# Kernel tuning notes

Hardware: AMD Instinct MI355X
Metric: run time of the kernel (lower is better)

## Reference

```python
import jax, jax.numpy as jnp
import numpy as np

LN_EPS = 1e-5
EPS = 1e-8
MESH_LR = 1.0
MESH_ITERS = 4
SH_ITERS = 5
SA_ITERS = 3


def build_grid(res):
    ranges = [np.linspace(0.0, 1.0, num=r) for r in res]
    g = np.stack(np.meshgrid(*ranges, indexing='ij'), axis=-1)
    g = g.reshape(res[0], res[1], -1)[None]
    return jnp.asarray(np.concatenate([g, 1.0 - g], axis=-1).astype(np.float32))  # [1,H,W,4]


def layer_norm(x, w, b):
    m = jnp.mean(x, axis=-1, keepdims=True)
    v = jnp.var(x, axis=-1, keepdims=True)
    return (x - m) * jax.lax.rsqrt(v + LN_EPS) * w + b


def l2norm(x):
    n = jnp.linalg.norm(x, axis=-1, keepdims=True)
    return x / jnp.maximum(n, 1e-12)  # matches F.normalize eps


def conv_relu(x, w, b, stride):
    y = jax.lax.conv_general_dilated(x, w, (stride, stride), [(2, 2), (2, 2)],
                                     dimension_numbers=('NCHW', 'OIHW', 'NCHW'))
    return jax.nn.relu(y + b[None, :, None, None])


def sinkhorn(C, a, b, u=None, v=None, n_iters=SH_ITERS):
    # log-domain Sinkhorn; C: [B,N,S] cost, a: [B,N], b: [B,S] marginals
    p = -C
    log_a, log_b = jnp.log(a), jnp.log(b)
    if u is None:
        u = jnp.zeros_like(a)
    if v is None:
        v = jnp.zeros_like(b)
    for _ in range(n_iters):
        u = log_a - jax.nn.logsumexp(p + v[:, None, :], axis=2)
        v = log_b - jax.nn.logsumexp(p + u[:, :, None], axis=1)
    pi = jnp.exp(p + u[:, :, None] + v[:, None, :])
    return pi, u, v


def minimize_entropy_of_sinkhorn(C0, a, b, mesh_lr=MESH_LR, n_mesh_iters=MESH_ITERS):
    # gradient descent on the cost matrix to minimize entropy of the transport plan
    def ent(C, u, v):
        pi, u2, v2 = sinkhorn(C, a, b, u=u, v=v)
        e = jnp.mean(-jnp.sum(pi * jnp.log(pi + EPS), axis=(1, 2)))
        return e, (u2, v2)

    grad_fn = jax.grad(ent, has_aux=True)
    u, v = jnp.zeros_like(a), jnp.zeros_like(b)
    C = C0
    for _ in range(n_mesh_iters):
        g, (u, v) = grad_fn(C, u, v)
        C = C - mesh_lr * g
    return C, u, v


def gru_cell(x, h, wih, whh, bih, bhh):
    gi = x @ wih.T + bih
    gh = h @ whh.T + bhh
    ir, iz, inn = jnp.split(gi, 3, axis=-1)
    hr, hz, hn = jnp.split(gh, 3, axis=-1)
    r = jax.nn.sigmoid(ir + hr)
    z = jax.nn.sigmoid(iz + hz)
    n = jnp.tanh(inn + r * hn)
    return (1.0 - z) * n + z * h


def setup_inputs() -> dict:
    key = jax.random.key(0)
    ks = iter(jax.random.split(key, 48))

    def nrm(shape, fan_in):
        return jax.random.normal(next(ks), shape, jnp.float32) / np.sqrt(fan_in).astype(np.float32)

    B, d, S, HID = 16, 64, 8, 128
    z = lambda *s: jnp.zeros(s, jnp.float32)
    o = lambda *s: jnp.ones(s, jnp.float32)
    inp = {
        'image': jax.random.normal(next(ks), (B, 3, 128, 128), jnp.float32),
        'slots_noise': jax.random.normal(next(ks), (B, S, d), jnp.float32),
        'conv1_w': nrm((64, 3, 5, 5), 75), 'conv1_b': z(64),
        'conv2_w': nrm((64, 64, 5, 5), 1600), 'conv2_b': z(64),
        'conv3_w': nrm((64, 64, 5, 5), 1600), 'conv3_b': z(64),
        'conv4_w': nrm((64, 64, 5, 5), 1600), 'conv4_b': z(64),
        'pos_w': nrm((d, 4), 4), 'pos_b': z(d),
        'mlp1_w': nrm((d, d), d), 'mlp1_b': z(d),
        'mlp2_w': nrm((d, d), d), 'mlp2_b': z(d),
        'ln_in_w': o(d), 'ln_in_b': z(d),
        'wk': nrm((d, d), d), 'wv': nrm((d, d), d), 'wq': nrm((d, d), d),
        'mwi_w': nrm((1, d), d), 'mwi_b': z(1),
        'mws_w': nrm((1, d), d), 'mws_b': z(1),
        'ln_sl_w': o(d), 'ln_sl_b': z(d),
        'gru_wih': nrm((3 * d, d), d), 'gru_whh': nrm((3 * d, d), d),
        'gru_bih': z(3 * d), 'gru_bhh': z(3 * d),
        'ln_ff_w': o(d), 'ln_ff_b': z(d),
        'fc1_w': nrm((HID, d), d), 'fc1_b': z(HID),
        'fc2_w': nrm((d, HID), HID), 'fc2_b': z(d),
        'slots_mu': nrm((1, 1, d), d),
        'slots_sigma': jax.random.uniform(next(ks), (1, 1, d), jnp.float32),
        'num_slots': 8,
    }
    return inp


def reference(image, slots_noise, conv1_w, conv1_b, conv2_w, conv2_b, conv3_w, conv3_b,
              conv4_w, conv4_b, pos_w, pos_b, mlp1_w, mlp1_b, mlp2_w, mlp2_b,
              ln_in_w, ln_in_b, wk, wv, wq, mwi_w, mwi_b, mws_w, mws_b,
              ln_sl_w, ln_sl_b, gru_wih, gru_whh, gru_bih, gru_bhh,
              ln_ff_w, ln_ff_b, fc1_w, fc1_b, fc2_w, fc2_b,
              slots_mu, slots_sigma, num_slots):
    B = image.shape[0]
    d = slots_mu.shape[-1]
    # --- CNN encoder (strided_convs=True => latent 32x32) ---
    x = conv_relu(image, conv1_w, conv1_b, 1)
    x = conv_relu(x, conv2_w, conv2_b, 2)
    x = conv_relu(x, conv3_w, conv3_b, 2)
    x = conv_relu(x, conv4_w, conv4_b, 1)          # [B,64,32,32]
    x = x.transpose(0, 2, 3, 1)                    # [B,32,32,64]
    grid = build_grid((32, 32))                    # [1,32,32,4]
    x = x + (grid @ pos_w.T + pos_b)               # soft position embed
    feat = x.reshape(B, -1, d)                     # [B,1024,64]
    # --- pre-slot-attention MLP ---
    feat = jax.nn.relu(feat @ mlp1_w.T + mlp1_b) @ mlp2_w.T + mlp2_b
    # --- slot attention with MESH-Sinkhorn ---
    n_s = num_slots
    slots = slots_mu + (jnp.abs(slots_sigma) + EPS) * slots_noise  # Normal rsample
    inp = layer_norm(feat, ln_in_w, ln_in_b)
    k = inp @ wk.T
    v = inp @ wv.T
    a = jax.nn.softmax((inp @ mwi_w.T + mwi_b).squeeze(-1), axis=-1) * n_s  # [B,N]
    kn = l2norm(k)
    attn = None
    for _ in range(SA_ITERS):
        slots_prev = slots
        s = layer_norm(slots, ln_sl_w, ln_sl_b)
        bm = jax.nn.softmax((s @ mws_w.T + mws_b).squeeze(-1), axis=-1) * n_s  # [B,S]
        q = s @ wq.T
        C = 1.0 - jnp.einsum('bnd,bsd->bns', kn, l2norm(q))  # cosine distance
        C, p, qq = minimize_entropy_of_sinkhorn(C, a, bm)
        pi, _, _ = sinkhorn(C, a, bm, u=p, v=qq)
        attn = pi.transpose(0, 2, 1)                         # [B,S,N]
        updates = jnp.einsum('bsn,bnd->bsd', attn, v)
        slots = gru_cell(updates.reshape(-1, d), slots_prev.reshape(-1, d),
                         gru_wih, gru_whh, gru_bih, gru_bhh).reshape(B, n_s, d)
        h = layer_norm(slots, ln_ff_w, ln_ff_b)
        slots = slots + (jax.nn.relu(h @ fc1_w.T + fc1_b) @ fc2_w.T + fc2_b)
    return slots, attn
```

## Files before the change

### kernel.cpp

```cpp
#include <hip/hip_runtime.h>
#include <hip/hip_bf16.h>


#define LN_EPS 1e-5f
#define SEPS 1e-8f
#define LN8 2.0794415416798357f

__device__ inline float ldf(float x) { return x; }
__device__ inline float ldf(__hip_bfloat16 x) { return __bfloat162float(x); }
__device__ inline void stf(float* p, float v) { *p = v; }
__device__ inline void stf(__hip_bfloat16* p, float v) { *p = __float2bfloat16(v); }

__device__ inline float wmaxall(float v) {
#pragma unroll
  for (int o = 32; o; o >>= 1) v = fmaxf(v, __shfl_down(v, o));
  return __shfl(v, 0);
}
__device__ inline float wsumall(float v) {
#pragma unroll
  for (int o = 32; o; o >>= 1) v += __shfl_down(v, o);
  return __shfl(v, 0);
}
__device__ inline int wsumi(int v) {
#pragma unroll
  for (int o = 32; o; o >>= 1) v += __shfl_down(v, o);
  return __shfl(v, 0);
}
__device__ inline float fast_sigmoid(float x) { return 1.f / (1.f + __expf(-x)); }
__device__ inline float fast_tanh(float x) { return 1.f - 2.f / (__expf(2.f * x) + 1.f); }

__global__ __launch_bounds__(64) void sniff_kernel(const unsigned int* __restrict__ img,
                                                   int* __restrict__ flag) {
  int cnt = 0;
  for (int i = threadIdx.x; i < 512; i += 64) {
    unsigned lo = img[i] & 0xFFFFu;
    int e = (int)((lo >> 7) & 0xFFu);
    cnt += (e >= 96 && e <= 140) ? 1 : 0;
  }
  cnt = wsumi(cnt);
  if (threadIdx.x == 0) *flag = (cnt >= 300) ? 1 : 0;
}

struct CvtArgs {
  const void* src[39];
  long off[40];
};

__global__ __launch_bounds__(256) void convert_kernel(CvtArgs a, const int* __restrict__ flag,
                                                      float* __restrict__ dst, long total) {
  const int isbf = *flag;
  for (long g = (long)blockIdx.x * 256 + threadIdx.x; g < total; g += (long)gridDim.x * 256) {
    int lo = 0, hi = 38;
    while (lo < hi) {
      int mid = (lo + hi + 1) >> 1;
      if (a.off[mid] <= g) lo = mid; else hi = mid - 1;
    }
    long li = g - a.off[lo];
    float v;
    if (isbf) v = __bfloat162float(((const __hip_bfloat16*)a.src[lo])[li]);
    else      v = ((const float*)a.src[lo])[li];
    dst[g] = v;
  }
}

struct TwArgs {
  long soff[9]; long doff[9]; int R[9]; int C[9];
};

__global__ __launch_bounds__(256) void transw_kernel(const float* __restrict__ cvt,
                                                     float* __restrict__ tws, TwArgs a) {
  int m = blockIdx.x;
  const float* S = cvt + a.soff[m];
  float* D = tws + a.doff[m];
  int R = a.R[m], C = a.C[m];
  for (int idx = threadIdx.x; idx < R * C; idx += 256) {
    int i = idx / C, j = idx - i * C;
    D[j * R + i] = S[idx];
  }
}

template <int S, typename TIN, typename TOUT>
__global__ __launch_bounds__(256) void conv5x5(
    const TIN* __restrict__ in, const float* __restrict__ wgt,
    const float* __restrict__ bias, TOUT* __restrict__ out,
    int Cin, int H, int W, int Ho, int Wo, int Cout, int tilesX) {
  constexpr int P = 15 * S + 5;
  constexpr int PP = (S == 1) ? 20 : 40;
  constexpr int NCH = (S == 1) ? 2 : 3;
  constexpr int NP = (P * P + 255) / 256;
  __shared__ __align__(16) float patch[P * PP];
  __shared__ float wt16[25 * 16];
  const int b = blockIdx.z;
  const int ocg = blockIdx.y * 16;
  const int ty0 = (blockIdx.x / tilesX) * 16, tx0 = (blockIdx.x % tilesX) * 16;
  const int og = threadIdx.x >> 6;
  const int r = (threadIdx.x >> 2) & 15;
  const int rx = threadIdx.x & 3;
  const int iy0 = ty0 * S - 2, ix0 = tx0 * S - 2;
  const long HW = (long)H * W;

  int toff[NP], soff[NP];
#pragma unroll
  for (int q = 0; q < NP; q++) {
    int idx = threadIdx.x + 256 * q;
    toff[q] = -1;
    soff[q] = -1;
    if (idx < P * P) {
      int py = idx / P, px = idx - py * P;
      int iy = iy0 + py, ix = ix0 + px;
      int pxs = (S == 2) ? (px ^ (((py >> 1) & 1) << 2)) : px;
      toff[q] = py * PP + pxs;
      if (iy >= 0 && iy < H && ix >= 0 && ix < W) soff[q] = iy * W + ix;
    }
  }
  int wsrc[2];
#pragma unroll
  for (int q = 0; q < 2; q++) {
    int idx = threadIdx.x + 256 * q;
    wsrc[q] = (idx < 400) ? (((ocg + (idx & 15)) * Cin) * 25 + (idx >> 4)) : -1;
  }

  float acc[4][4];
#pragma unroll
  for (int p = 0; p < 4; p++)
#pragma unroll
    for (int j = 0; j < 4; j++) acc[p][j] = 0.f;

  float pr[NP], wr[2];
  {
    const TIN* inp = in + (long)b * Cin * HW;
#pragma unroll
    for (int q = 0; q < NP; q++) pr[q] = (soff[q] >= 0) ? ldf(inp[soff[q]]) : 0.f;
#pragma unroll
    for (int q = 0; q < 2; q++) wr[q] = (wsrc[q] >= 0) ? wgt[wsrc[q]] : 0.f;
  }

  for (int ci = 0; ci < Cin; ++ci) {
    __syncthreads();
#pragma unroll
    for (int q = 0; q < NP; q++)
      if (toff[q] >= 0) patch[toff[q]] = pr[q];
#pragma unroll
    for (int q = 0; q < 2; q++) {
      int idx = threadIdx.x + 256 * q;
      if (idx < 400) wt16[idx] = wr[q];
    }
    __syncthreads();
    if (ci + 1 < Cin) {
      const TIN* inp = in + ((long)b * Cin + ci + 1) * HW;
#pragma unroll
      for (int q = 0; q < NP; q++) pr[q] = (soff[q] >= 0) ? ldf(inp[soff[q]]) : 0.f;
#pragma unroll
      for (int q = 0; q < 2; q++)
        if (wsrc[q] >= 0) wr[q] = wgt[wsrc[q] + (ci + 1) * 25];
    }
#pragma unroll
    for (int ky = 0; ky < 5; ky++) {
      float win[4 * NCH];
      const int row = r * S + ky;
      const float* rb = &patch[row * PP];
      if constexpr (S == 2) {
        const int sw = (row >> 1) & 1;
#pragma unroll
        for (int c = 0; c < NCH; c++) {
          const int g = rx * 2 + c;
          float4 t4 = *(const float4*)(rb + ((g ^ sw) << 2));
          win[4 * c + 0] = t4.x;
          win[4 * c + 1] = t4.y;
          win[4 * c + 2] = t4.z;
          win[4 * c + 3] = t4.w;
        }
      } else {
        const float* bp = rb + rx * 4;
#pragma unroll
        for (int c = 0; c < NCH; c++) {
          float4 t4 = *(const float4*)(bp + 4 * c);
          win[4 * c + 0] = t4.x;
          win[4 * c + 1] = t4.y;
          win[4 * c + 2] = t4.z;
          win[4 * c + 3] = t4.w;
        }
      }
#pragma unroll
      for (int kx = 0; kx < 5; kx++) {
        const float4 wv = *(const float4*)&wt16[(ky * 5 + kx) * 16 + og * 4];
#pragma unroll
        for (int p = 0; p < 4; p++) {
          float iv = win[p * S + kx];
          acc[p][0] += iv * wv.x;
          acc[p][1] += iv * wv.y;
          acc[p][2] += iv * wv.z;
          acc[p][3] += iv * wv.w;
        }
      }
    }
  }
  const int oy = ty0 + r, ox0 = tx0 + rx * 4;
#pragma unroll
  for (int j = 0; j < 4; j++) {
    int oc = ocg + og * 4 + j;
    float bs = bias[oc];
    TOUT* op = &out[(((long)b * Cout + oc) * Ho + oy) * Wo + ox0];
#pragma unroll
    for (int p = 0; p < 4; p++) stf(&op[p], fmaxf(acc[p][j] + bs, 0.f));
  }
}

__global__ __launch_bounds__(64) void token_kernel(
    const float* __restrict__ act4, const float* __restrict__ pos_w,
    const float* __restrict__ pos_b,
    const float* __restrict__ mlp1T, const float* __restrict__ mlp1_b,
    const float* __restrict__ mlp2T, const float* __restrict__ mlp2_b,
    const float* __restrict__ lnin_w, const float* __restrict__ lnin_b,
    const float* __restrict__ wkT, const float* __restrict__ wvT,
    const float* __restrict__ mwi_w, const float* __restrict__ mwi_b,
    float* __restrict__ knT_out, float* __restrict__ v_out, float* __restrict__ lg_out) {
  const int t = blockIdx.x, i = threadIdx.x;
  const int b = t >> 10, nn = t & 1023;
  const int h = nn >> 5, w = nn & 31;
  __shared__ float f[64], h1[64], inp[64];
  {
    float gh = h * (1.f / 31.f), gw = w * (1.f / 31.f);
    float e = gh * pos_w[i * 4 + 0] + gw * pos_w[i * 4 + 1] +
              (1.f - gh) * pos_w[i * 4 + 2] + (1.f - gw) * pos_w[i * 4 + 3] + pos_b[i];
    f[i] = act4[(((long)b * 64 + i) * 32 + h) * 32 + w] + e;
  }
  __syncthreads();
  float acc = 0.f;
  for (int j = 0; j < 64; j++) acc += f[j] * mlp1T[j * 64 + i];
  h1[i] = fmaxf(acc + mlp1_b[i], 0.f);
  __syncthreads();
  acc = 0.f;
  for (int j = 0; j < 64; j++) acc += h1[j] * mlp2T[j * 64 + i];
  float x = acc + mlp2_b[i];
  float m = wsumall(x) * (1.f / 64.f);
  float d0 = x - m;
  float var = wsumall(d0 * d0) * (1.f / 64.f);
  float xin = d0 * rsqrtf(var + LN_EPS) * lnin_w[i] + lnin_b[i];
  inp[i] = xin;
  __syncthreads();
  float kv = 0.f, vv = 0.f;
  for (int j = 0; j < 64; j++) {
    float ij = inp[j];
    kv += ij * wkT[j * 64 + i];
    vv += ij * wvT[j * 64 + i];
  }
  float ss = wsumall(kv * kv);
  knT_out[(long)b * 65536 + i * 1024 + nn] = kv / fmaxf(sqrtf(ss), 1e-12f);
  v_out[(long)t * 64 + i] = vv;
  float lg = wsumall(xin * mwi_w[i]);
  if (i == 0) lg_out[t] = lg + mwi_b[0];
}

__global__ __launch_bounds__(512) void sa_kernel(
    const float* __restrict__ knT_g, const float* __restrict__ v_g,
    const float* __restrict__ la_g, const float* __restrict__ noise,
    const float* __restrict__ mu_w, const float* __restrict__ sg_w,
    const float* __restrict__ lnsl_w, const float* __restrict__ lnsl_b,
    const float* __restrict__ mws_w, const float* __restrict__ mws_b,
    const float* __restrict__ wqT,
    const float* __restrict__ wihT, const float* __restrict__ whhT,
    const float* __restrict__ bih, const float* __restrict__ bhh,
    const float* __restrict__ lnff_w, const float* __restrict__ lnff_b,
    const float* __restrict__ fc1T, const float* __restrict__ fc1_b,
    const float* __restrict__ fc2T, const float* __restrict__ fc2_b,
    float* __restrict__ out) {
  const int b = blockIdx.x, tid = threadIdx.x;
  const int wv = tid >> 6, ln = tid & 63;

  __shared__ float sCt[8192];
  __shared__ float sEc[8192];
  __shared__ float sLa[1024], sELa[1024], sHid[1024];
  __shared__ float sPart[512 * 9];
  __shared__ float sVh[48], sV[8], sEsv[8], sGv[8], sLb[8], sBm[8];
  __shared__ float sC1[8], sEvh[8];
  __shared__ float sSlots[512], sNorm[512], sQn[512], sUpd[512];

  const float* knt = knT_g + (long)b * 65536;
  const float* vf = v_g + (long)b * 65536;
  float sInvH[5][2];
  float gPr[2][8];
  float gInit[2];

  {
    int dd = tid & 63;
    sSlots[tid] = mu_w[dd] + (fabsf(sg_w[dd]) + SEPS) * noise[(long)b * 512 + tid];
  }
  for (int n = tid; n < 1024; n += 512) sLa[n] = la_g[b * 1024 + n];
  __syncthreads();
  {
    float a0 = sLa[tid], a1 = sLa[tid + 512];
    float m0 = wmaxall(fmaxf(a0, a1));
    if (ln == 0) sBm[wv] = m0;
    __syncthreads();
    float M = sBm[0];
#pragma unroll
    for (int s = 1; s < 8; s++) M = fmaxf(M, sBm[s]);
    float e0 = wsumall(__expf(a0 - M) + __expf(a1 - M));
    if (ln == 0) sGv[wv] = e0;
    __syncthreads();
    float SS = 0.f;
#pragma unroll
    for (int s = 0; s < 8; s++) SS += sGv[s];
    float lse = M + __logf(SS);
    float l0 = a0 - lse + LN8, l1 = a1 - lse + LN8;
    sLa[tid] = l0;
    sLa[tid + 512] = l1;
    sELa[tid] = __expf(l0);
    sELa[tid + 512] = __expf(l1);
  }
  __syncthreads();

  for (int it = 0; it < 3; ++it) {
    {
      float x = sSlots[wv * 64 + ln];
      float m = wsumall(x) * (1.f / 64.f);
      float d0 = x - m;
      float var = wsumall(d0 * d0) * (1.f / 64.f);
      float xn = d0 * rsqrtf(var + LN_EPS) * lnsl_w[ln] + lnsl_b[ln];
      sNorm[wv * 64 + ln] = xn;
      float bmv = wsumall(xn * mws_w[ln]);
      if (ln == 0) sBm[wv] = bmv + mws_b[0];
    }
    __syncthreads();
    if (tid == 0) {
      float mx = -1e30f;
      for (int s = 0; s < 8; s++) mx = fmaxf(mx, sBm[s]);
      float ss = 0.f;
      for (int s = 0; s < 8; s++) ss += __expf(sBm[s] - mx);
      float lse = mx + __logf(ss);
      for (int s = 0; s < 8; s++) sLb[s] = sBm[s] - lse + LN8;
    }
    {
      float acc = 0.f;
      for (int j = 0; j < 64; j++) acc += sNorm[wv * 64 + j] * wqT[j * 64 + ln];
      sQn[tid] = acc;
    }
    __syncthreads();
    {
      float qv = sQn[wv * 64 + ln];
      float ss = wsumall(qv * qv);
      sQn[wv * 64 + ln] = qv / fmaxf(sqrtf(ss), 1e-12f);
    }
    if (tid < 8) {
      sV[tid] = 0.f;
      sEsv[tid] = 1.f;
    }
    __syncthreads();

#pragma unroll
    for (int k = 0; k < 2; k++) {
      int n = tid + 512 * k;
      float acc[8];
#pragma unroll
      for (int s = 0; s < 8; s++) acc[s] = 0.f;
      for (int j = 0; j < 64; j++) {
        float kvv = knt[j * 1024 + n];
#pragma unroll
        for (int s = 0; s < 8; s++) acc[s] += kvv * sQn[s * 64 + j];
      }
#pragma unroll
      for (int s = 0; s < 8; s++) {
        float c = 1.f - acc[s];
        sCt[s * 1024 + n] = c;
        sEc[s * 1024 + n] = __expf(-c);
      }
    }
    __syncthreads();

    for (int m = 0; m < 4; m++) {
#pragma unroll
      for (int t = 1; t <= 5; t++) {
        if (t == 1 && tid < 8) sVh[tid] = sV[tid];
        float esv_r[8], part[8];
#pragma unroll
        for (int s = 0; s < 8; s++) { esv_r[s] = sEsv[s]; part[s] = 0.f; }
#pragma unroll
        for (int k = 0; k < 2; k++) {
          int n = tid + 512 * k;
          float ec[8], S = 0.f;
#pragma unroll
          for (int s = 0; s < 8; s++) {
            ec[s] = sEc[s * 1024 + n];
            S += esv_r[s] * ec[s];
          }
          float inv = 1.f / S;
          sInvH[t - 1][k] = inv;
          float w = sELa[n] * inv;
#pragma unroll
          for (int s = 0; s < 8; s++) part[s] += w * ec[s];
        }
#pragma unroll
        for (int s = 0; s < 8; s++) sPart[tid * 9 + s] = part[s];
        __syncthreads();
        {
          int s = wv;
          float acc = 0.f;
#pragma unroll
          for (int q = 0; q < 8; q++) acc += sPart[(ln + 64 * q) * 9 + s];
          acc = wsumall(acc);
          if (ln == 0) {
            float vs = sLb[s] - __logf(acc);
            sV[s] = vs;
            sVh[t * 8 + s] = vs;
            sEsv[s] = __expf(vs);
          }
        }
        __syncthreads();
      }
      {
        float esv_r[8], part[8];
#pragma unroll
        for (int s = 0; s < 8; s++) { esv_r[s] = sEsv[s]; part[s] = 0.f; }
#pragma unroll
        for (int k = 0; k < 2; k++) {
          int n = tid + 512 * k;
          float al = sELa[n] * sInvH[4][k];
          float gul = 0.f;
#pragma unroll
          for (int s = 0; s < 8; s++) {
            float pi = al * esv_r[s] * sEc[s * 1024 + n];
            float gl = -(__logf(pi + SEPS) + pi / (pi + SEPS)) * pi * (1.f / 16.f);
            gPr[k][s] = gl;
            gul += gl;
            part[s] += gl;
          }
          gInit[k] = gul;
        }
#pragma unroll
        for (int s = 0; s < 8; s++) sPart[tid * 9 + s] = part[s];
        __syncthreads();
        {
          int s = wv;
          float acc = 0.f;
#pragma unroll
          for (int q = 0; q < 8; q++) acc += sPart[(ln + 64 * q) * 9 + s];
          acc = wsumall(acc);
          if (ln == 0) {
            sGv[s] = acc;
            sC1[s] = acc * __expf(sVh[40 + s] - sLb[s]);
            sEvh[s] = __expf(sVh[32 + s]);
          }
        }
        __syncthreads();
      }
#pragma unroll
      for (int t = 5; t >= 1; t--) {
        float c1_r[8], evh_r[8], part[8];
#pragma unroll
        for (int s = 0; s < 8; s++) {
          c1_r[s] = sC1[s];
          evh_r[s] = sEvh[s];
          part[s] = 0.f;
        }
#pragma unroll
        for (int k = 0; k < 2; k++) {
          int n = tid + 512 * k;
          float inv = sInvH[t - 1][k];
          float al = sELa[n] * inv;
          float gul = (t == 5) ? gInit[k] : 0.f;
          float ec[8];
#pragma unroll
          for (int s = 0; s < 8; s++) {
            ec[s] = sEc[s * 1024 + n];
            float t2 = al * c1_r[s] * ec[s];
            gPr[k][s] -= t2;
            gul -= t2;
          }
          float bv = gul * inv;
#pragma unroll
          for (int s = 0; s < 8; s++) {
            float pe = bv * ec[s];
            gPr[k][s] -= pe * evh_r[s];
            part[s] += pe;
          }
          if (t == 1) {
#pragma unroll
            for (int s = 0; s < 8; s++) {
              float cn = sCt[s * 1024 + n] + gPr[k][s];
              sCt[s * 1024 + n] = cn;
              sEc[s * 1024 + n] = __expf(-cn);
            }
          }
        }
        if (t > 1) {
#pragma unroll
          for (int s = 0; s < 8; s++) sPart[tid * 9 + s] = part[s];
        }
        if (t == 1 && tid < 8) {
          float vs = sVh[40 + tid];
          sV[tid] = vs;
          sEsv[tid] = __expf(vs);
        }
        __syncthreads();
        if (t > 1) {
          int s = wv;
          float acc = 0.f;
#pragma unroll
          for (int q = 0; q < 8; q++) acc += sPart[(ln + 64 * q) * 9 + s];
          acc = wsumall(acc);
          if (ln == 0) {
            float gn = -sEvh[s] * acc;
            sGv[s] = gn;
            sC1[s] = gn * __expf(sVh[(t - 1) * 8 + s] - sLb[s]);
            sEvh[s] = __expf(sVh[(t - 2) * 8 + s]);
          }
          __syncthreads();
        }
      }
    }

    float invF[2];
    for (int t = 0; t < 5; t++) {
      float esv_r[8], part[8];
#pragma unroll
      for (int s = 0; s < 8; s++) { esv_r[s] = sEsv[s]; part[s] = 0.f; }
#pragma unroll
      for (int k = 0; k < 2; k++) {
        int n = tid + 512 * k;
        float ec[8], S = 0.f;
#pragma unroll
        for (int s = 0; s < 8; s++) {
          ec[s] = sEc[s * 1024 + n];
          S += esv_r[s] * ec[s];
        }
        float inv = 1.f / S;
        invF[k] = inv;
        float w = sELa[n] * inv;
#pragma unroll
        for (int s = 0; s < 8; s++) part[s] += w * ec[s];
      }
#pragma unroll
      for (int s = 0; s < 8; s++) sPart[tid * 9 + s] = part[s];
      __syncthreads();
      {
        int s = wv;
        float acc = 0.f;
#pragma unroll
        for (int q = 0; q < 8; q++) acc += sPart[(ln + 64 * q) * 9 + s];
        acc = wsumall(acc);
        if (ln == 0) {
          float vs = sLb[s] - __logf(acc);
          sV[s] = vs;
          sEsv[s] = __expf(vs);
        }
      }
      __syncthreads();
    }
    {
      float esv_r[8];
#pragma unroll
      for (int s = 0; s < 8; s++) esv_r[s] = sEsv[s];
#pragma unroll
      for (int k = 0; k < 2; k++) {
        int n = tid + 512 * k;
        float al = sELa[n] * invF[k];
#pragma unroll
        for (int s = 0; s < 8; s++)
          sCt[s * 1024 + n] = al * esv_r[s] * sEc[s * 1024 + n];
      }
    }
    __syncthreads();
    if (it == 2) {
      for (int o = tid; o < 8192; o += 512) out[8192 + (long)b * 8192 + o] = sCt[o];
    }
    {
      int s = tid >> 6, dd = tid & 63;
      float acc = 0.f;
      for (int n = 0; n < 1024; n++) acc += sCt[s * 1024 + n] * vf[n * 64 + dd];
      sUpd[tid] = acc;
    }
    __syncthreads();
    float newslot;
    {
      int s = tid >> 6, i = tid & 63;
      const float* x = &sUpd[s * 64];
      const float* h = &sSlots[s * 64];
      float gir = 0, giz = 0, gin = 0, ghr = 0, ghz = 0, ghn = 0;
      for (int j = 0; j < 64; j++) {
        float xv = x[j], hv = h[j];
        gir += xv * wihT[j * 192 + i];
        giz += xv * wihT[j * 192 + 64 + i];
        gin += xv * wihT[j * 192 + 128 + i];
        ghr += hv * whhT[j * 192 + i];
        ghz += hv * whhT[j * 192 + 64 + i];
        ghn += hv * whhT[j * 192 + 128 + i];
      }
      gir += bih[i]; giz += bih[64 + i]; gin += bih[128 + i];
      ghr += bhh[i]; ghz += bhh[64 + i]; ghn += bhh[128 + i];
      float r = fast_sigmoid(gir + ghr);
      float z = fast_sigmoid(giz + ghz);
      float nn = fast_tanh(gin + r * ghn);
      newslot = (1.f - z) * nn + z * h[i];
    }
    __syncthreads();
    sSlots[tid] = newslot;
    __syncthreads();
    {
      float x = sSlots[wv * 64 + ln];
      float m = wsumall(x) * (1.f / 64.f);
      float d0 = x - m;
      float var = wsumall(d0 * d0) * (1.f / 64.f);
      sNorm[wv * 64 + ln] = d0 * rsqrtf(var + LN_EPS) * lnff_w[ln] + lnff_b[ln];
    }
    __syncthreads();
    for (int o = tid; o < 1024; o += 512) {
      int s = o >> 7, k2 = o & 127;
      float acc = 0.f;
      for (int j = 0; j < 64; j++) acc += sNorm[s * 64 + j] * fc1T[j * 128 + k2];
      sHid[o] = fmaxf(acc + fc1_b[k2], 0.f);
    }
    __syncthreads();
    {
      int s = tid >> 6, i = tid & 63;
      float acc = 0.f;
      for (int j = 0; j < 128; j++) acc += sHid[s * 128 + j] * fc2T[j * 64 + i];
      newslot = sSlots[tid] + acc + fc2_b[i];
    }
    __syncthreads();
    sSlots[tid] = newslot;
    __syncthreads();
  }
  out[(long)b * 512 + tid] = sSlots[tid];
}

extern "C" void kernel_launch(void* const* d_in, const int* in_sizes, int n_in,
                              void* d_out, int out_size, void* d_ws, size_t ws_size,
                              hipStream_t stream) {
  (void)n_in; (void)out_size; (void)ws_size;
  char* ws = (char*)d_ws;
  float* cvt  = (float*)ws;
  float* lgts = (float*)(ws + 5570560ull);
  __hip_bfloat16* act1 = (__hip_bfloat16*)(ws + 5636096ull);
  __hip_bfloat16* act2 = (__hip_bfloat16*)(ws + 39190528ull);
  float* act3 = (float*)(ws + 5636096ull);
  float* act4 = (float*)(ws + 9830400ull);
  float* knT  = (float*)(ws + 14024704ull);
  float* vf   = (float*)(ws + 18219008ull);
  int*   flag = (int*)(ws + 47579136ull);
  float* tws  = (float*)(ws + 47583232ull);

  CvtArgs ca;
  long total = 0;
  for (int i = 0; i < 39; i++) { ca.src[i] = d_in[i]; ca.off[i] = total; total += in_sizes[i]; }
  ca.off[39] = total;

  sniff_kernel<<<1, 64, 0, stream>>>((const unsigned int*)d_in[0], flag);
  convert_kernel<<<1024, 256, 0, stream>>>(ca, flag, cvt, total);

#define ARR(i) (cvt + ca.off[i])
  TwArgs ta;
  {
    const int src[9] = {12, 14, 18, 19, 20, 27, 28, 33, 35};
    const int R[9] = {64, 64, 64, 64, 64, 192, 192, 128, 64};
    const int C[9] = {64, 64, 64, 64, 64, 64, 64, 64, 128};
    long d = 0;
    for (int m2 = 0; m2 < 9; m2++) {
      ta.soff[m2] = ca.off[src[m2]];
      ta.doff[m2] = d;
      ta.R[m2] = R[m2];
      ta.C[m2] = C[m2];
      d += (long)R[m2] * C[m2];
    }
  }
  transw_kernel<<<9, 256, 0, stream>>>(cvt, tws, ta);
  float* mlp1T = tws + 0,     *mlp2T = tws + 4096,  *wkT = tws + 8192, *wvT = tws + 12288;
  float* wqT   = tws + 16384, *wihT  = tws + 20480, *whhT = tws + 32768;
  float* fc1T  = tws + 45056, *fc2T  = tws + 53248;

  const float* image = ARR(0);
  const float* noise = ARR(1);

  conv5x5<1, float, __hip_bfloat16><<<dim3(64, 4, 16), 256, 0, stream>>>(
      image, ARR(2), ARR(3), act1, 3, 128, 128, 128, 128, 64, 8);
  conv5x5<2, __hip_bfloat16, __hip_bfloat16><<<dim3(16, 4, 16), 256, 0, stream>>>(
      act1, ARR(4), ARR(5), act2, 64, 128, 128, 64, 64, 64, 4);
  conv5x5<2, __hip_bfloat16, float><<<dim3(4, 4, 16), 256, 0, stream>>>(
      act2, ARR(6), ARR(7), act3, 64, 64, 64, 32, 32, 64, 2);
  conv5x5<1, float, float><<<dim3(4, 4, 16), 256, 0, stream>>>(
      act3, ARR(8), ARR(9), act4, 64, 32, 32, 32, 32, 64, 2);

  token_kernel<<<16384, 64, 0, stream>>>(act4, ARR(10), ARR(11),
                                         mlp1T, ARR(13), mlp2T, ARR(15),
                                         ARR(16), ARR(17), wkT, wvT, ARR(21), ARR(22),
                                         knT, vf, lgts);

  sa_kernel<<<16, 512, 0, stream>>>(knT, vf, lgts, noise, ARR(37), ARR(38),
                                    ARR(25), ARR(26), ARR(23), ARR(24), wqT,
                                    wihT, whhT, ARR(29), ARR(30),
                                    ARR(31), ARR(32), fc1T, ARR(34), fc2T, ARR(36),
                                    (float*)d_out);
#undef ARR
}
```

Measured before the change: 942.5 us.

## Batch four tokens per block with shared-memory weights; fold dtype sniff into convert

The token kernel now handles four tokens per 256-thread block and stages the four 64x64 weight matrices (mlp1, mlp2, wk, wv) in shared memory, so the matvecs read LDS instead of global/L2. This is meant to cut repeated global weight reads and per-block launch overhead across 16384 tiny blocks. The cost is a 64KB+ shared-memory copy per block, which limits occupancy and is paid 4096 times. Separately, the dtype-sniff kernel is merged into the convert kernel: every block recomputes the flag itself, which removes one launch.

Result: no change. 947.7 us (+0.6%).

```diff
diff --git a/kernel.cpp b/kernel.cpp
--- a/kernel.cpp
+++ b/kernel.cpp
@@ -29,26 +29,29 @@
 __device__ inline float fast_sigmoid(float x) { return 1.f / (1.f + __expf(-x)); }
 __device__ inline float fast_tanh(float x) { return 1.f - 2.f / (__expf(2.f * x) + 1.f); }
 
-__global__ __launch_bounds__(64) void sniff_kernel(const unsigned int* __restrict__ img,
-                                                   int* __restrict__ flag) {
-  int cnt = 0;
-  for (int i = threadIdx.x; i < 512; i += 64) {
-    unsigned lo = img[i] & 0xFFFFu;
-    int e = (int)((lo >> 7) & 0xFFu);
-    cnt += (e >= 96 && e <= 140) ? 1 : 0;
-  }
-  cnt = wsumi(cnt);
-  if (threadIdx.x == 0) *flag = (cnt >= 300) ? 1 : 0;
-}
-
 struct CvtArgs {
   const void* src[39];
   long off[40];
 };
 
-__global__ __launch_bounds__(256) void convert_kernel(CvtArgs a, const int* __restrict__ flag,
+__global__ __launch_bounds__(256) void convert_kernel(CvtArgs a,
                                                       float* __restrict__ dst, long total) {
-  const int isbf = *flag;
+  __shared__ int sFlag;
+  {
+    const unsigned int* img = (const unsigned int*)a.src[0];
+    if (threadIdx.x < 64) {
+      int cnt = 0;
+      for (int i = threadIdx.x; i < 512; i += 64) {
+        unsigned lo = img[i] & 0xFFFFu;
+        int e = (int)((lo >> 7) & 0xFFu);
+        cnt += (e >= 96 && e <= 140) ? 1 : 0;
+      }
+      cnt = wsumi(cnt);
+      if (threadIdx.x == 0) sFlag = (cnt >= 300) ? 1 : 0;
+    }
+    __syncthreads();
+  }
+  const int isbf = sFlag;
   for (long g = (long)blockIdx.x * 256 + threadIdx.x; g < total; g += (long)gridDim.x * 256) {
     int lo = 0, hi = 38;
     while (lo < hi) {
@@ -206,7 +209,7 @@
   }
 }
 
-__global__ __launch_bounds__(64) void token_kernel(
+__global__ __launch_bounds__(256) void token_kernel(
     const float* __restrict__ act4, const float* __restrict__ pos_w,
     const float* __restrict__ pos_b,
     const float* __restrict__ mlp1T, const float* __restrict__ mlp1_b,
@@ -215,35 +218,43 @@
     const float* __restrict__ wkT, const float* __restrict__ wvT,
     const float* __restrict__ mwi_w, const float* __restrict__ mwi_b,
     float* __restrict__ knT_out, float* __restrict__ v_out, float* __restrict__ lg_out) {
-  const int t = blockIdx.x, i = threadIdx.x;
+  const int wq = threadIdx.x >> 6, i = threadIdx.x & 63;
+  const int t = blockIdx.x * 4 + wq;
   const int b = t >> 10, nn = t & 1023;
   const int h = nn >> 5, w = nn & 31;
-  __shared__ float f[64], h1[64], inp[64];
+  __shared__ float sM1[4096], sM2[4096], sWk[4096], sWv[4096];
+  __shared__ float f[4][64], h1[4][64], inp[4][64];
+  for (int idx = threadIdx.x; idx < 4096; idx += 256) {
+    sM1[idx] = mlp1T[idx];
+    sM2[idx] = mlp2T[idx];
+    sWk[idx] = wkT[idx];
+    sWv[idx] = wvT[idx];
+  }
   {
     float gh = h * (1.f / 31.f), gw = w * (1.f / 31.f);
     float e = gh * pos_w[i * 4 + 0] + gw * pos_w[i * 4 + 1] +
               (1.f - gh) * pos_w[i * 4 + 2] + (1.f - gw) * pos_w[i * 4 + 3] + pos_b[i];
-    f[i] = act4[(((long)b * 64 + i) * 32 + h) * 32 + w] + e;
+    f[wq][i] = act4[(((long)b * 64 + i) * 32 + h) * 32 + w] + e;
   }
   __syncthreads();
   float acc = 0.f;
-  for (int j = 0; j < 64; j++) acc += f[j] * mlp1T[j * 64 + i];
-  h1[i] = fmaxf(acc + mlp1_b[i], 0.f);
+  for (int j = 0; j < 64; j++) acc += f[wq][j] * sM1[j * 64 + i];
+  h1[wq][i] = fmaxf(acc + mlp1_b[i], 0.f);
   __syncthreads();
   acc = 0.f;
-  for (int j = 0; j < 64; j++) acc += h1[j] * mlp2T[j * 64 + i];
+  for (int j = 0; j < 64; j++) acc += h1[wq][j] * sM2[j * 64 + i];
   float x = acc + mlp2_b[i];
   float m = wsumall(x) * (1.f / 64.f);
   float d0 = x - m;
   float var = wsumall(d0 * d0) * (1.f / 64.f);
   float xin = d0 * rsqrtf(var + LN_EPS) * lnin_w[i] + lnin_b[i];
-  inp[i] = xin;
+  inp[wq][i] = xin;
   __syncthreads();
   float kv = 0.f, vv = 0.f;
   for (int j = 0; j < 64; j++) {
-    float ij = inp[j];
-    kv += ij * wkT[j * 64 + i];
-    vv += ij * wvT[j * 64 + i];
+    float ij = inp[wq][j];
+    kv += ij * sWk[j * 64 + i];
+    vv += ij * sWv[j * 64 + i];
   }
   float ss = wsumall(kv * kv);
   knT_out[(long)b * 65536 + i * 1024 + nn] = kv / fmaxf(sqrtf(ss), 1e-12f);
@@ -637,7 +648,6 @@
   float* act4 = (float*)(ws + 9830400ull);
   float* knT  = (float*)(ws + 14024704ull);
   float* vf   = (float*)(ws + 18219008ull);
-  int*   flag = (int*)(ws + 47579136ull);
   float* tws  = (float*)(ws + 47583232ull);
 
   CvtArgs ca;
@@ -645,8 +655,7 @@
   for (int i = 0; i < 39; i++) { ca.src[i] = d_in[i]; ca.off[i] = total; total += in_sizes[i]; }
   ca.off[39] = total;
 
-  sniff_kernel<<<1, 64, 0, stream>>>((const unsigned int*)d_in[0], flag);
-  convert_kernel<<<1024, 256, 0, stream>>>(ca, flag, cvt, total);
+  convert_kernel<<<1024, 256, 0, stream>>>(ca, cvt, total);
 
 #define ARR(i) (cvt + ca.off[i])
   TwArgs ta;
@@ -680,7 +689,7 @@
   conv5x5<1, float, float><<<dim3(4, 4, 16), 256, 0, stream>>>(
       act3, ARR(8), ARR(9), act4, 64, 32, 32, 32, 32, 64, 2);
 
-  token_kernel<<<16384, 64, 0, stream>>>(act4, ARR(10), ARR(11),
+  token_kernel<<<4096, 256, 0, stream>>>(act4, ARR(10), ARR(11),
                                          mlp1T, ARR(13), mlp2T, ARR(15),
                                          ARR(16), ARR(17), wkT, wvT, ARR(21), ARR(22),
                                          knT, vf, lgts);
```
